# Performance work log

Hardware: AMD Instinct MI355X
Metric: run time of the kernel (lower is better)

Reference implementation:

```python
import jax, jax.numpy as jnp
import numpy as np

N_NODES = 50000


def setup_inputs() -> dict:
    key = jax.random.key(0)
    k1, k2, k3, k4, k5, k6 = jax.random.split(key, 6)
    N, E, D, F = 50000, 800000, 512, 256
    feature_ori = jax.random.normal(k1, (N, D), dtype=jnp.float32)
    feature_aug = jax.random.normal(k2, (N, D), dtype=jnp.float32)
    edge_row = jax.random.randint(k3, (E,), 0, N, dtype=jnp.int32)
    edge_col = jax.random.randint(k4, (E,), 0, N, dtype=jnp.int32)
    edge_val = jax.random.uniform(k5, (E,), dtype=jnp.float32)
    # kaiming-uniform-ish init for weight, zeros for bias (as in reset_parameters)
    bound = float(np.sqrt(6.0 / D))
    weight = jax.random.uniform(k6, (D, F), dtype=jnp.float32, minval=-bound, maxval=bound)
    bias = jnp.zeros((F,), dtype=jnp.float32)
    return {
        "feature_ori": feature_ori,
        "feature_aug": feature_aug,
        "edge_row": edge_row,
        "edge_col": edge_col,
        "edge_val": edge_val,
        "weight": weight,
        "bias": bias,
    }


def _branch(feat, weight, bias, edge_row, edge_col, edge_val):
    # support = X @ W  -> [N, F]
    support = feat @ weight
    # sparse aggregation: out[i] = sum_{e: row[e]=i} val[e] * support[col[e]]
    msgs = edge_val[:, None] * support[edge_col]          # [E, F]
    out = jax.ops.segment_sum(msgs, edge_row, num_segments=N_NODES)
    return jax.nn.relu(out + bias)


def reference(feature_ori, feature_aug, edge_row, edge_col, edge_val, weight, bias):
    out_ori = _branch(feature_ori, weight, bias, edge_row, edge_col, edge_val)
    out_aug = _branch(feature_aug, weight, bias, edge_row, edge_col, edge_val)
    return (out_ori, out_aug)
```

## Files before the change

kernel.cpp:

```cpp
#include <hip/hip_runtime.h>
#include <hip/hip_bf16.h>

#define NNODES 50000
#define NEDGES 800000
#define DIN    512
#define FOUT   256

typedef __attribute__((ext_vector_type(8))) short short8;
typedef __attribute__((ext_vector_type(4))) float f32x4;
typedef __attribute__((ext_vector_type(4))) unsigned short usv4;

static __device__ __forceinline__ unsigned short f2bf(float f) {
    unsigned int u = __float_as_uint(f);
    u += 0x7FFF + ((u >> 16) & 1);
    return (unsigned short)(u >> 16);
}
static __device__ __forceinline__ float bf2f(unsigned short h) {
    return __uint_as_float(((unsigned int)h) << 16);
}

__global__ void wt_convert(const float* __restrict__ W, unsigned short* __restrict__ Wt) {
    int o = blockIdx.x * 256 + threadIdx.x;
    int n = o >> 9, k = o & 511;
    Wt[o] = f2bf(W[k * FOUT + n]);
}

__global__ void hist_kernel(const int* __restrict__ row, int* __restrict__ cnt) {
    int e = blockIdx.x * 256 + threadIdx.x;
    if (e < NEDGES) atomicAdd(&cnt[row[e]], 1);
}

__global__ void scan_partial(const int* __restrict__ cnt, int* __restrict__ partial) {
    __shared__ int sm[256];
    int i = blockIdx.x * 256 + threadIdx.x;
    int v = (i < NNODES) ? cnt[i] : 0;
    sm[threadIdx.x] = v; __syncthreads();
    for (int s = 128; s > 0; s >>= 1) {
        if (threadIdx.x < s) sm[threadIdx.x] += sm[threadIdx.x + s];
        __syncthreads();
    }
    if (threadIdx.x == 0) partial[blockIdx.x] = sm[0];
}

__global__ void scan_exclusive_small(int* __restrict__ partial, int nb) {
    __shared__ int sm[256];
    int t = threadIdx.x;
    int v = (t < nb) ? partial[t] : 0;
    sm[t] = v; __syncthreads();
    for (int off = 1; off < 256; off <<= 1) {
        int add = (t >= off) ? sm[t - off] : 0;
        __syncthreads();
        sm[t] += add;
        __syncthreads();
    }
    if (t < nb) partial[t] = sm[t] - v;
}

__global__ void scan_write(const int* __restrict__ cnt, const int* __restrict__ partial,
                           int* __restrict__ row_start) {
    __shared__ int sm[256];
    int t = threadIdx.x;
    int i = blockIdx.x * 256 + t;
    int v = (i < NNODES) ? cnt[i] : 0;
    sm[t] = v; __syncthreads();
    for (int off = 1; off < 256; off <<= 1) {
        int add = (t >= off) ? sm[t - off] : 0;
        __syncthreads();
        sm[t] += add;
        __syncthreads();
    }
    if (i < NNODES) row_start[i] = partial[blockIdx.x] + sm[t] - v;
    if (i == 0) row_start[NNODES] = NEDGES;
}

__global__ void scatter_kernel(const int* __restrict__ row, const int* __restrict__ row_start,
                               int* __restrict__ cursor, int* __restrict__ perm) {
    int e = blockIdx.x * 256 + threadIdx.x;
    if (e < NEDGES) {
        int r = row[e];
        int pos = atomicAdd(&cursor[r], 1);
        perm[row_start[r] + pos] = e;
    }
}

__global__ __launch_bounds__(256, 2)
void gemm_kernel(const float* __restrict__ Xo, const float* __restrict__ Xa,
                 const unsigned short* __restrict__ Wt,
                 unsigned short* __restrict__ So, unsigned short* __restrict__ Sa) {
    __shared__ __align__(16) unsigned short As[128][32];
    __shared__ __align__(16) unsigned short Bs[128][32];
    const int tid = threadIdx.x;
    const float* __restrict__ X = blockIdx.z ? Xa : Xo;
    unsigned short* __restrict__ S = blockIdx.z ? Sa : So;
    const int m_base = blockIdx.x * 128;
    const int n_base = blockIdx.y * 128;
    const int lane = tid & 63, wave = tid >> 6;
    const int wm = (wave >> 1) * 64, wn = (wave & 1) * 64;
    const int quad = lane >> 4, r16 = lane & 15;

    f32x4 acc[4][4] = {};

    const int colf  = (tid & 7) * 4;
    const int rbase = tid >> 3;
    const int kseg  = (tid & 3) * 8;
    const int nrow  = tid >> 2;

    for (int k0 = 0; k0 < DIN; k0 += 32) {
        #pragma unroll
        for (int i = 0; i < 4; i++) {
            int rr = i * 32 + rbase;
            int gm = m_base + rr;
            float4 v = (gm < NNODES) ? *(const float4*)&X[(long)gm * DIN + k0 + colf]
                                     : make_float4(0.f, 0.f, 0.f, 0.f);
            usv4 h;
            h.x = f2bf(v.x); h.y = f2bf(v.y); h.z = f2bf(v.z); h.w = f2bf(v.w);
            *(usv4*)&As[rr][colf] = h;
        }
        #pragma unroll
        for (int i = 0; i < 2; i++) {
            int nn = i * 64 + nrow;
            *(uint4*)&Bs[nn][kseg] =
                *(const uint4*)&Wt[(long)(n_base + nn) * DIN + k0 + kseg];
        }
        __syncthreads();

        short8 a_frag[4], b_frag[4];
        #pragma unroll
        for (int mi = 0; mi < 4; mi++)
            a_frag[mi] = *(const short8*)&As[wm + mi * 16 + r16][quad * 8];
        #pragma unroll
        for (int ni = 0; ni < 4; ni++)
            b_frag[ni] = *(const short8*)&Bs[wn + ni * 16 + r16][quad * 8];
        #pragma unroll
        for (int mi = 0; mi < 4; mi++)
            #pragma unroll
            for (int ni = 0; ni < 4; ni++)
                acc[mi][ni] = __builtin_amdgcn_mfma_f32_16x16x32_bf16(
                    a_frag[mi], b_frag[ni], acc[mi][ni], 0, 0, 0);
        __syncthreads();
    }

    #pragma unroll
    for (int mi = 0; mi < 4; mi++) {
        #pragma unroll
        for (int rr = 0; rr < 4; rr++) {
            int m = m_base + wm + mi * 16 + quad * 4 + rr;
            if (m < NNODES) {
                #pragma unroll
                for (int ni = 0; ni < 4; ni++) {
                    int n = n_base + wn + ni * 16 + r16;
                    S[(long)m * FOUT + n] = f2bf(acc[mi][ni][rr]);
                }
            }
        }
    }
}

__global__ __launch_bounds__(256)
void aggregate_kernel(const int* __restrict__ row_start, const int* __restrict__ perm,
                      const int* __restrict__ col, const float* __restrict__ val,
                      const unsigned short* __restrict__ So,
                      const unsigned short* __restrict__ Sa,
                      const float* __restrict__ bias, float* __restrict__ out) {
    int node = blockIdx.x * 4 + (threadIdx.x >> 6);
    int lane = threadIdx.x & 63;
    if (node >= NNODES) return;
    int s = row_start[node], e = row_start[node + 1];
    float ao0 = 0.f, ao1 = 0.f, ao2 = 0.f, ao3 = 0.f;
    float aa0 = 0.f, aa1 = 0.f, aa2 = 0.f, aa3 = 0.f;
    for (int idx = s; idx < e; idx++) {
        int ed = perm[idx];
        int c = col[ed];
        float v = val[ed];
        usv4 po = *(const usv4*)&So[(long)c * FOUT + lane * 4];
        usv4 pa = *(const usv4*)&Sa[(long)c * FOUT + lane * 4];
        ao0 += v * bf2f(po.x); ao1 += v * bf2f(po.y);
        ao2 += v * bf2f(po.z); ao3 += v * bf2f(po.w);
        aa0 += v * bf2f(pa.x); aa1 += v * bf2f(pa.y);
        aa2 += v * bf2f(pa.z); aa3 += v * bf2f(pa.w);
    }
    float4 b = *(const float4*)&bias[lane * 4];
    long o = (long)node * FOUT + lane * 4;
    float4 ro, ra;
    ro.x = fmaxf(ao0 + b.x, 0.f); ro.y = fmaxf(ao1 + b.y, 0.f);
    ro.z = fmaxf(ao2 + b.z, 0.f); ro.w = fmaxf(ao3 + b.w, 0.f);
    ra.x = fmaxf(aa0 + b.x, 0.f); ra.y = fmaxf(aa1 + b.y, 0.f);
    ra.z = fmaxf(aa2 + b.z, 0.f); ra.w = fmaxf(aa3 + b.w, 0.f);
    *(float4*)&out[o] = ro;
    *(float4*)&out[(long)NNODES * FOUT + o] = ra;
}

extern "C" void kernel_launch(void* const* d_in, const int* in_sizes, int n_in,
                              void* d_out, int out_size, void* d_ws, size_t ws_size,
                              hipStream_t stream) {
    const float* Xo   = (const float*)d_in[0];
    const float* Xa   = (const float*)d_in[1];
    const int*   erow = (const int*)d_in[2];
    const int*   ecol = (const int*)d_in[3];
    const float* eval_= (const float*)d_in[4];
    const float* W    = (const float*)d_in[5];
    const float* bias = (const float*)d_in[6];
    float* out = (float*)d_out;

    char* ws = (char*)d_ws;
    unsigned short* So        = (unsigned short*)(ws);
    unsigned short* Sa        = (unsigned short*)(ws + 25600000);
    unsigned short* Wt        = (unsigned short*)(ws + 51200000);
    int*            cnt       = (int*)(ws + 51462144);
    int*            cursor    = (int*)(ws + 51662144);
    int*            row_start = (int*)(ws + 51862144);
    int*            partial   = (int*)(ws + 52062208);
    int*            perm      = (int*)(ws + 52063232);

    (void)in_sizes; (void)n_in; (void)out_size; (void)ws_size;

    hipMemsetAsync(cnt, 0, 400000, stream);

    wt_convert<<<512, 256, 0, stream>>>(W, Wt);
    hist_kernel<<<3125, 256, 0, stream>>>(erow, cnt);
    scan_partial<<<196, 256, 0, stream>>>(cnt, partial);
    scan_exclusive_small<<<1, 256, 0, stream>>>(partial, 196);
    scan_write<<<196, 256, 0, stream>>>(cnt, partial, row_start);
    scatter_kernel<<<3125, 256, 0, stream>>>(erow, row_start, cursor, perm);

    dim3 gg(391, 2, 2);
    gemm_kernel<<<gg, 256, 0, stream>>>(Xo, Xa, Wt, So, Sa);

    aggregate_kernel<<<12500, 256, 0, stream>>>(row_start, perm, ecol, eval_,
                                                So, Sa, bias, out);
}
```

Measured before the change: 553.0 us.

## Pack edge col and bf16 value into CSR, interleave branch supports, widen GEMM tile

The scatter step now writes a packed 32-bit word per edge into CSR order: a 16-bit column index plus the edge value rounded to bf16. This removes the perm, col and val indirection chain in aggregation. The two branch support matrices are interleaved into one [N,512] buffer, so each neighbour's ori and aug rows sit next to each other, and the aggregation loop is unrolled by four to keep more gathers in flight. The GEMM now uses 512-thread blocks covering all 256 output columns, with padded LDS rows to reduce bank conflicts. The trade-offs are bf16 rounding of edge values and a packing scheme that only works while N is below 65536; the scatter cursor is also now reset before use.

```diff
diff --git a/kernel.cpp b/kernel.cpp
--- a/kernel.cpp
+++ b/kernel.cpp
@@ -73,29 +73,32 @@
     if (i == 0) row_start[NNODES] = NEDGES;
 }
 
-__global__ void scatter_kernel(const int* __restrict__ row, const int* __restrict__ row_start,
-                               int* __restrict__ cursor, int* __restrict__ perm) {
+__global__ void scatter_kernel(const int* __restrict__ row, const int* __restrict__ col,
+                               const float* __restrict__ val,
+                               const int* __restrict__ row_start,
+                               int* __restrict__ cursor, unsigned int* __restrict__ cv) {
     int e = blockIdx.x * 256 + threadIdx.x;
     if (e < NEDGES) {
         int r = row[e];
         int pos = atomicAdd(&cursor[r], 1);
-        perm[row_start[r] + pos] = e;
-    }
-}
-
-__global__ __launch_bounds__(256, 2)
+        unsigned int vb = f2bf(val[e]);
+        cv[row_start[r] + pos] = (vb << 16) | (unsigned int)col[e];
+    }
+}
+
+__global__ __launch_bounds__(512, 2)
 void gemm_kernel(const float* __restrict__ Xo, const float* __restrict__ Xa,
                  const unsigned short* __restrict__ Wt,
-                 unsigned short* __restrict__ So, unsigned short* __restrict__ Sa) {
-    __shared__ __align__(16) unsigned short As[128][32];
-    __shared__ __align__(16) unsigned short Bs[128][32];
+                 unsigned short* __restrict__ S) {
+    __shared__ __align__(16) unsigned short As[128][40];
+    __shared__ __align__(16) unsigned short Bs[256][40];
     const int tid = threadIdx.x;
-    const float* __restrict__ X = blockIdx.z ? Xa : Xo;
-    unsigned short* __restrict__ S = blockIdx.z ? Sa : So;
+    const int branch = blockIdx.z;
+    const float* __restrict__ X = branch ? Xa : Xo;
+    const int boff = branch * 256;
     const int m_base = blockIdx.x * 128;
-    const int n_base = blockIdx.y * 128;
     const int lane = tid & 63, wave = tid >> 6;
-    const int wm = (wave >> 1) * 64, wn = (wave & 1) * 64;
+    const int wm = (wave >> 2) * 64, wn = (wave & 3) * 64;
     const int quad = lane >> 4, r16 = lane & 15;
 
     f32x4 acc[4][4] = {};
@@ -107,8 +110,8 @@
 
     for (int k0 = 0; k0 < DIN; k0 += 32) {
         #pragma unroll
-        for (int i = 0; i < 4; i++) {
-            int rr = i * 32 + rbase;
+        for (int i = 0; i < 2; i++) {
+            int rr = i * 64 + rbase;
             int gm = m_base + rr;
             float4 v = (gm < NNODES) ? *(const float4*)&X[(long)gm * DIN + k0 + colf]
                                      : make_float4(0.f, 0.f, 0.f, 0.f);
@@ -118,9 +121,9 @@
         }
         #pragma unroll
         for (int i = 0; i < 2; i++) {
-            int nn = i * 64 + nrow;
+            int nn = i * 128 + nrow;
             *(uint4*)&Bs[nn][kseg] =
-                *(const uint4*)&Wt[(long)(n_base + nn) * DIN + k0 + kseg];
+                *(const uint4*)&Wt[(long)nn * DIN + k0 + kseg];
         }
         __syncthreads();
 
@@ -148,8 +151,8 @@
             if (m < NNODES) {
                 #pragma unroll
                 for (int ni = 0; ni < 4; ni++) {
-                    int n = n_base + wn + ni * 16 + r16;
-                    S[(long)m * FOUT + n] = f2bf(acc[mi][ni][rr]);
+                    int n = wn + ni * 16 + r16;
+                    S[(long)m * 512 + boff + n] = f2bf(acc[mi][ni][rr]);
                 }
             }
         }
@@ -157,10 +160,9 @@
 }
 
 __global__ __launch_bounds__(256)
-void aggregate_kernel(const int* __restrict__ row_start, const int* __restrict__ perm,
-                      const int* __restrict__ col, const float* __restrict__ val,
-                      const unsigned short* __restrict__ So,
-                      const unsigned short* __restrict__ Sa,
+void aggregate_kernel(const int* __restrict__ row_start,
+                      const unsigned int* __restrict__ cv,
+                      const unsigned short* __restrict__ S,
                       const float* __restrict__ bias, float* __restrict__ out) {
     int node = blockIdx.x * 4 + (threadIdx.x >> 6);
     int lane = threadIdx.x & 63;
@@ -168,19 +170,44 @@
     int s = row_start[node], e = row_start[node + 1];
     float ao0 = 0.f, ao1 = 0.f, ao2 = 0.f, ao3 = 0.f;
     float aa0 = 0.f, aa1 = 0.f, aa2 = 0.f, aa3 = 0.f;
-    for (int idx = s; idx < e; idx++) {
-        int ed = perm[idx];
-        int c = col[ed];
-        float v = val[ed];
-        usv4 po = *(const usv4*)&So[(long)c * FOUT + lane * 4];
-        usv4 pa = *(const usv4*)&Sa[(long)c * FOUT + lane * 4];
-        ao0 += v * bf2f(po.x); ao1 += v * bf2f(po.y);
-        ao2 += v * bf2f(po.z); ao3 += v * bf2f(po.w);
-        aa0 += v * bf2f(pa.x); aa1 += v * bf2f(pa.y);
-        aa2 += v * bf2f(pa.z); aa3 += v * bf2f(pa.w);
-    }
-    float4 b = *(const float4*)&bias[lane * 4];
-    long o = (long)node * FOUT + lane * 4;
+    const int lo = lane * 4;
+
+    int idx = s;
+    for (; idx + 4 <= e; idx += 4) {
+        unsigned int w0 = cv[idx], w1 = cv[idx + 1], w2 = cv[idx + 2], w3 = cv[idx + 3];
+        const unsigned short* p0 = &S[(long)(w0 & 0xFFFFu) * 512 + lo];
+        const unsigned short* p1 = &S[(long)(w1 & 0xFFFFu) * 512 + lo];
+        const unsigned short* p2 = &S[(long)(w2 & 0xFFFFu) * 512 + lo];
+        const unsigned short* p3 = &S[(long)(w3 & 0xFFFFu) * 512 + lo];
+        usv4 po0 = *(const usv4*)p0;       usv4 pa0 = *(const usv4*)(p0 + 256);
+        usv4 po1 = *(const usv4*)p1;       usv4 pa1 = *(const usv4*)(p1 + 256);
+        usv4 po2 = *(const usv4*)p2;       usv4 pa2 = *(const usv4*)(p2 + 256);
+        usv4 po3 = *(const usv4*)p3;       usv4 pa3 = *(const usv4*)(p3 + 256);
+        float v0 = bf2f((unsigned short)(w0 >> 16));
+        float v1 = bf2f((unsigned short)(w1 >> 16));
+        float v2 = bf2f((unsigned short)(w2 >> 16));
+        float v3 = bf2f((unsigned short)(w3 >> 16));
+        ao0 += v0 * bf2f(po0.x); ao1 += v0 * bf2f(po0.y); ao2 += v0 * bf2f(po0.z); ao3 += v0 * bf2f(po0.w);
+        aa0 += v0 * bf2f(pa0.x); aa1 += v0 * bf2f(pa0.y); aa2 += v0 * bf2f(pa0.z); aa3 += v0 * bf2f(pa0.w);
+        ao0 += v1 * bf2f(po1.x); ao1 += v1 * bf2f(po1.y); ao2 += v1 * bf2f(po1.z); ao3 += v1 * bf2f(po1.w);
+        aa0 += v1 * bf2f(pa1.x); aa1 += v1 * bf2f(pa1.y); aa2 += v1 * bf2f(pa1.z); aa3 += v1 * bf2f(pa1.w);
+        ao0 += v2 * bf2f(po2.x); ao1 += v2 * bf2f(po2.y); ao2 += v2 * bf2f(po2.z); ao3 += v2 * bf2f(po2.w);
+        aa0 += v2 * bf2f(pa2.x); aa1 += v2 * bf2f(pa2.y); aa2 += v2 * bf2f(pa2.z); aa3 += v2 * bf2f(pa2.w);
+        ao0 += v3 * bf2f(po3.x); ao1 += v3 * bf2f(po3.y); ao2 += v3 * bf2f(po3.z); ao3 += v3 * bf2f(po3.w);
+        aa0 += v3 * bf2f(pa3.x); aa1 += v3 * bf2f(pa3.y); aa2 += v3 * bf2f(pa3.z); aa3 += v3 * bf2f(pa3.w);
+    }
+    for (; idx < e; idx++) {
+        unsigned int w = cv[idx];
+        const unsigned short* p = &S[(long)(w & 0xFFFFu) * 512 + lo];
+        usv4 po = *(const usv4*)p;
+        usv4 pa = *(const usv4*)(p + 256);
+        float v = bf2f((unsigned short)(w >> 16));
+        ao0 += v * bf2f(po.x); ao1 += v * bf2f(po.y); ao2 += v * bf2f(po.z); ao3 += v * bf2f(po.w);
+        aa0 += v * bf2f(pa.x); aa1 += v * bf2f(pa.y); aa2 += v * bf2f(pa.z); aa3 += v * bf2f(pa.w);
+    }
+
+    float4 b = *(const float4*)&bias[lo];
+    long o = (long)node * FOUT + lo;
     float4 ro, ra;
     ro.x = fmaxf(ao0 + b.x, 0.f); ro.y = fmaxf(ao1 + b.y, 0.f);
     ro.z = fmaxf(ao2 + b.z, 0.f); ro.w = fmaxf(ao3 + b.w, 0.f);
@@ -203,29 +230,26 @@
     float* out = (float*)d_out;
 
     char* ws = (char*)d_ws;
-    unsigned short* So        = (unsigned short*)(ws);
-    unsigned short* Sa        = (unsigned short*)(ws + 25600000);
+    unsigned short* S         = (unsigned short*)(ws);
     unsigned short* Wt        = (unsigned short*)(ws + 51200000);
     int*            cnt       = (int*)(ws + 51462144);
-    int*            cursor    = (int*)(ws + 51662144);
-    int*            row_start = (int*)(ws + 51862144);
-    int*            partial   = (int*)(ws + 52062208);
-    int*            perm      = (int*)(ws + 52063232);
+    int*            row_start = (int*)(ws + 51662144);
+    int*            partial   = (int*)(ws + 51862208);
+    unsigned int*   cv        = (unsigned int*)(ws + 51863232);
 
     (void)in_sizes; (void)n_in; (void)out_size; (void)ws_size;
 
-    hipMemsetAsync(cnt, 0, 400000, stream);
-
+    hipMemsetAsync(cnt, 0, 200000, stream);
     wt_convert<<<512, 256, 0, stream>>>(W, Wt);
     hist_kernel<<<3125, 256, 0, stream>>>(erow, cnt);
     scan_partial<<<196, 256, 0, stream>>>(cnt, partial);
     scan_exclusive_small<<<1, 256, 0, stream>>>(partial, 196);
     scan_write<<<196, 256, 0, stream>>>(cnt, partial, row_start);
-    scatter_kernel<<<3125, 256, 0, stream>>>(erow, row_start, cursor, perm);
-
-    dim3 gg(391, 2, 2);
-    gemm_kernel<<<gg, 256, 0, stream>>>(Xo, Xa, Wt, So, Sa);
-
-    aggregate_kernel<<<12500, 256, 0, stream>>>(row_start, perm, ecol, eval_,
-                                                So, Sa, bias, out);
-}
+    hipMemsetAsync(cnt, 0, 200000, stream);
+    scatter_kernel<<<3125, 256, 0, stream>>>(erow, ecol, eval_, row_start, cnt, cv);
+
+    dim3 gg(391, 1, 2);
+    gemm_kernel<<<gg, 512, 0, stream>>>(Xo, Xa, Wt, S);
+
+    aggregate_kernel<<<12500, 256, 0, stream>>>(row_start, cv, S, bias, out);
+}
```

Result: faster. 484.2 us (-12.4%).
